# Optimization experiments

Hardware: AMD Instinct MI355X
Metric: run time of the kernel (lower is better)

Reference implementation:

```python
import jax, jax.numpy as jnp
import numpy as np

B, T, E, A = 4, 4096, 512, 64

def setup_inputs() -> dict:
    key = jax.random.key(0)
    k1, k2, k3, k4 = jax.random.split(key, 4)
    embedded = jax.random.normal(k1, (B, T, E), dtype=jnp.float32)
    # torch Linear(E, A, bias=False): weight [A, E], y = x @ W.T. Store as [E, A].
    s = 1.0 / np.sqrt(E)
    Wq = jax.random.uniform(k2, (E, A), dtype=jnp.float32, minval=-s, maxval=s)
    Wk = jax.random.uniform(k3, (E, A), dtype=jnp.float32, minval=-s, maxval=s)
    Wv = jax.random.uniform(k4, (E, A), dtype=jnp.float32, minval=-s, maxval=s)
    return {"embedded": embedded, "Wq": Wq, "Wk": Wk, "Wv": Wv}

def reference(embedded, Wq, Wk, Wv):
    Q = embedded @ Wq  # [B, T, A]
    K = embedded @ Wk
    V = embedded @ Wv
    A_dim = V.shape[-1]
    scores = jnp.einsum('btd,bsd->bts', Q, K) / jnp.sqrt(jnp.float32(A_dim))  # [B, T, T]
    Tlen = scores.shape[-1]
    causal = jnp.tril(jnp.ones((Tlen, Tlen), dtype=bool))
    scores = jnp.where(causal, scores, -jnp.inf)
    attn = jax.nn.softmax(scores, axis=-1)
    out = jnp.einsum('bts,bsd->btd', attn, V)  # [B, T, A]
    return jnp.round(out, 4)
```

## Files before the change

### kernel.cpp

```cpp
#include <hip/hip_runtime.h>

#define B_ 4
#define T_ 4096
#define E_ 512
#define A_ 64
#define SQSCALE 0.1803368801111204f

typedef __attribute__((ext_vector_type(8)))  short bf16x8;
typedef __attribute__((ext_vector_type(8)))  unsigned short ushort8;
typedef __attribute__((ext_vector_type(4)))  unsigned int   u32x4;
typedef __attribute__((ext_vector_type(4)))  float f32x4;
typedef __attribute__((ext_vector_type(16))) float f32x16;

__device__ __forceinline__ unsigned short f2bf(float x) {
    union { float f; unsigned int u; } v; v.f = x;
    unsigned int r = v.u + 0x7fffu + ((v.u >> 16) & 1u);
    return (unsigned short)(r >> 16);
}
__device__ __forceinline__ unsigned cvtpk(float a, float b) {
    unsigned r;
    asm("v_cvt_pk_bf16_f32 %0, %1, %2" : "=v"(r) : "v"(a), "v"(b));
    return r;
}
__device__ __forceinline__ void pls(unsigned &a, unsigned &b) {
    asm("v_permlane32_swap_b32 %0, %1" : "+v"(a), "+v"(b));
}

__global__ __launch_bounds__(256) void prep_w(
    const float* __restrict__ Wq, const float* __restrict__ Wk,
    const float* __restrict__ Wv, unsigned short* __restrict__ Wp)
{
    const int e = blockIdx.x * 256 + threadIdx.x;
    const int nt = e >> 10;
    const int ks = (e >> 6) & 15;
    const int l  = e & 63;
    const int col = nt * 16 + (l & 15);
    const int kb  = ks * 32 + (l >> 4) * 8;
    const float* W = (col < 64) ? Wq : ((col < 128) ? Wk : Wv);
    const int cc = col & 63;
    const float sc = (col < 64) ? SQSCALE : 1.f;
    union { unsigned short s[8]; ushort8 v; } u;
    #pragma unroll
    for (int j = 0; j < 8; ++j) u.s[j] = f2bf(W[(kb + j) * 64 + cc] * sc);
    *(ushort8*)&Wp[(size_t)e * 8] = u.v;
}

__global__ __launch_bounds__(768, 4) void qkv_proj_kernel(
    const float* __restrict__ emb, const unsigned short* __restrict__ Wp,
    unsigned short* __restrict__ Qp, unsigned short* __restrict__ Kp,
    unsigned short* __restrict__ Vp)
{
    __shared__ unsigned short at[32][536];
    __shared__ unsigned short qt[32][72];
    __shared__ unsigned short kt[32][72];
    __shared__ unsigned short vt[64][40];
    const int tid = threadIdx.x;
    const long row0 = (long)blockIdx.x * 32;

    if (tid < 512) {
        const int r = tid >> 4, c16 = tid & 15;
        const float* __restrict__ src = emb + (row0 + r) * 512;
        #pragma unroll
        for (int j = 0; j < 4; ++j) {
            const int col = j * 128 + c16 * 8;
            const float4 x0 = *(const float4*)(src + col);
            const float4 x1 = *(const float4*)(src + col + 4);
            u32x4 p;
            p[0] = cvtpk(x0.x, x0.y); p[1] = cvtpk(x0.z, x0.w);
            p[2] = cvtpk(x1.x, x1.y); p[3] = cvtpk(x1.z, x1.w);
            *(u32x4*)&at[r][col] = p;
        }
    }
    __syncthreads();

    const int w = tid >> 6, lane = tid & 63;
    const int c = lane & 15, hi = lane >> 4;

    f32x4 acc[2];
    acc[0] = (f32x4){0.f, 0.f, 0.f, 0.f};
    acc[1] = (f32x4){0.f, 0.f, 0.f, 0.f};

    #pragma unroll
    for (int ks = 0; ks < 16; ++ks) {
        const bf16x8 bf_ = *(const bf16x8*)&Wp[((size_t)(w * 16 + ks) * 64 + lane) * 8];
        const bf16x8 a0 = *(const bf16x8*)&at[c][ks * 32 + hi * 8];
        const bf16x8 a1 = *(const bf16x8*)&at[16 + c][ks * 32 + hi * 8];
        acc[0] = __builtin_amdgcn_mfma_f32_16x16x32_bf16(a0, bf_, acc[0], 0, 0, 0);
        acc[1] = __builtin_amdgcn_mfma_f32_16x16x32_bf16(a1, bf_, acc[1], 0, 0, 0);
    }

    #pragma unroll
    for (int rr = 0; rr < 2; ++rr)
        #pragma unroll
        for (int r4 = 0; r4 < 4; ++r4) {
            const int rloc = rr * 16 + hi * 4 + r4;
            const unsigned short v = f2bf(acc[rr][r4]);
            if (w < 4)       qt[rloc][w * 16 + c] = v;
            else if (w < 8)  kt[rloc][(w - 4) * 16 + c] = v;
            else             vt[(w - 8) * 16 + c][rloc] = v;
        }
    __syncthreads();

    const int tloc = (int)(row0 & 4095);
    const long bb = row0 >> 12;
    const int ci  = tloc >> 6;
    const int f_  = (tloc >> 5) & 1;
    const int ks0 = (tloc >> 4) & 3;
    const int tt  = tloc >> 5;
    if (tid < 256) {
        const int kk = tid >> 6, l = tid & 63;
        const ushort8 kval = *(const ushort8*)&kt[l & 31][kk * 16 + (l >> 5) * 8];
        *(ushort8*)&Kp[((((bb * 64 + ci) * 2 + f_) * 4 + kk) * 64 + l) * 8] = kval;
        const ushort8 qval = *(const ushort8*)&qt[l & 31][kk * 16 + (l >> 5) * 8];
        *(ushort8*)&Qp[(((bb * 128 + tt) * 4 + kk) * 64 + l) * 8] = qval;
    } else if (tid < 512) {
        const int e = tid - 256;
        const int ksl = e >> 7, ct = (e >> 6) & 1, l = e & 63;
        const ushort8 val = *(const ushort8*)&vt[ct * 32 + (l & 31)][ksl * 16 + (l >> 5) * 8];
        *(ushort8*)&Vp[((((bb * 64 + ci) * 4 + ks0 + ksl) * 2 + ct) * 64 + l) * 8] = val;
    }
}

__global__ __launch_bounds__(512, 1) void attn_kernel(
    const unsigned short* __restrict__ Qp, const unsigned short* __restrict__ Kp,
    const unsigned short* __restrict__ Vp, float* __restrict__ out)
{
    __shared__ float accbuf[8][32][68];
    __shared__ float mbuf[8][32], lbuf[8][32];

    const int tid = threadIdx.x, w = tid >> 6, lane = tid & 63;
    const int c = lane & 31, h = lane >> 5;
    const int b = blockIdx.x & 3;
    const int pp = blockIdx.x >> 2;

    const unsigned short* __restrict__ Qpb = Qp + (size_t)b * 128 * 4 * 512;
    const unsigned short* __restrict__ Kpb = Kp + (size_t)b * 64 * 8 * 512;
    const unsigned short* __restrict__ Vpb = Vp + (size_t)b * 64 * 8 * 512;

    for (int ti = 0; ti < 2; ++ti) {
        const int t = ti ? pp : (127 - pp);
        const int qb = t << 5;
        const int nc = ((qb + 31) >> 6) + 1;

        bf16x8 qf[4];
        #pragma unroll
        for (int kk = 0; kk < 4; ++kk)
            qf[kk] = *(const bf16x8*)&Qpb[(((size_t)t * 4 + kk) * 64 + lane) * 8];

        f32x16 acc[2];
        #pragma unroll
        for (int ct = 0; ct < 2; ++ct)
            #pragma unroll
            for (int j = 0; j < 16; ++j) acc[ct][j] = 0.f;
        float m = -1e30f, l = 0.f;

        const unsigned short* kptr = Kpb + (size_t)w * 4096 + lane * 8;
        const unsigned short* vptr = Vpb + (size_t)w * 4096 + lane * 8;

        bf16x8 kf[2][4];
        {
            const unsigned short* kp0 = (w < nc) ? kptr : (kptr - (size_t)(w - nc + 1) * 4096);
            #pragma unroll
            for (int f = 0; f < 2; ++f)
                #pragma unroll
                for (int kk = 0; kk < 4; ++kk)
                    kf[f][kk] = *(const bf16x8*)&kp0[f * 2048 + kk * 512];
        }

        for (int ci = w; ci < nc; ci += 8) {
            const int s0 = ci << 6;

            bf16x8 vf[4][2];
            #pragma unroll
            for (int ks = 0; ks < 4; ++ks)
                #pragma unroll
                for (int ct = 0; ct < 2; ++ct)
                    vf[ks][ct] = *(const bf16x8*)&vptr[ks * 1024 + ct * 512];

            f32x16 sf[2];
            #pragma unroll
            for (int f = 0; f < 2; ++f)
                #pragma unroll
                for (int j = 0; j < 16; ++j) sf[f][j] = 0.f;
            __builtin_amdgcn_s_setprio(1);
            #pragma unroll
            for (int f = 0; f < 2; ++f)
                #pragma unroll
                for (int kk = 0; kk < 4; ++kk)
                    sf[f] = __builtin_amdgcn_mfma_f32_32x32x16_bf16(kf[f][kk], qf[kk], sf[f], 0, 0, 0);
            __builtin_amdgcn_s_setprio(0);

            const unsigned short* knp = (ci + 8 < nc) ? (kptr + 32768) : kptr;
            bf16x8 kn[2][4];
            #pragma unroll
            for (int f = 0; f < 2; ++f)
                #pragma unroll
                for (int kk = 0; kk < 4; ++kk)
                    kn[f][kk] = *(const bf16x8*)&knp[f * 2048 + kk * 512];

            if (s0 + 63 > qb) {
                #pragma unroll
                for (int f = 0; f < 2; ++f)
                    #pragma unroll
                    for (int r = 0; r < 16; ++r) {
                        const int key = s0 + f * 32 + ((r & 3) + 8 * (r >> 2)) + 4 * h;
                        if (key > qb + c) sf[f][r] = -1e30f;
                    }
            }

            float t0 = fmaxf(sf[0][0], sf[1][0]);
            float t1 = fmaxf(sf[0][1], sf[1][1]);
            float t2 = fmaxf(sf[0][2], sf[1][2]);
            float t3 = fmaxf(sf[0][3], sf[1][3]);
            #pragma unroll
            for (int r = 4; r < 16; r += 4) {
                t0 = fmaxf(t0, fmaxf(sf[0][r],     sf[1][r]));
                t1 = fmaxf(t1, fmaxf(sf[0][r + 1], sf[1][r + 1]));
                t2 = fmaxf(t2, fmaxf(sf[0][r + 2], sf[1][r + 2]));
                t3 = fmaxf(t3, fmaxf(sf[0][r + 3], sf[1][r + 3]));
            }
            float pm = fmaxf(fmaxf(t0, t1), fmaxf(t2, t3));
            pm = fmaxf(pm, __shfl_xor(pm, 32));

            float mn = m;
            if (__any(pm > m)) {
                mn = fmaxf(m, pm);
                const float sc = exp2f(m - mn);
                m = mn;
                l *= sc;
                #pragma unroll
                for (int ct = 0; ct < 2; ++ct)
                    #pragma unroll
                    for (int r = 0; r < 16; ++r) acc[ct][r] *= sc;
            }

            float s0a = 0.f, s1a = 0.f, s2a = 0.f, s3a = 0.f;
            #pragma unroll
            for (int f = 0; f < 2; ++f)
                #pragma unroll
                for (int r = 0; r < 16; r += 4) {
                    float p0 = exp2f(sf[f][r] - mn);
                    float p1 = exp2f(sf[f][r + 1] - mn);
                    float p2 = exp2f(sf[f][r + 2] - mn);
                    float p3 = exp2f(sf[f][r + 3] - mn);
                    sf[f][r] = p0; sf[f][r + 1] = p1; sf[f][r + 2] = p2; sf[f][r + 3] = p3;
                    s0a += p0; s1a += p1; s2a += p2; s3a += p3;
                }
            float rs = (s0a + s1a) + (s2a + s3a);
            rs += __shfl_xor(rs, 32);
            l += rs;

            #pragma unroll
            for (int f = 0; f < 2; ++f) {
                unsigned w01 = cvtpk(sf[f][0], sf[f][1]);
                unsigned w23 = cvtpk(sf[f][2], sf[f][3]);
                unsigned w45 = cvtpk(sf[f][4], sf[f][5]);
                unsigned w67 = cvtpk(sf[f][6], sf[f][7]);
                pls(w01, w45); pls(w23, w67);
                union { unsigned uu[4]; bf16x8 v; } pa0, pa1;
                pa0.uu[0] = w01; pa0.uu[1] = w23; pa0.uu[2] = w45; pa0.uu[3] = w67;
                unsigned x01 = cvtpk(sf[f][8],  sf[f][9]);
                unsigned x23 = cvtpk(sf[f][10], sf[f][11]);
                unsigned x45 = cvtpk(sf[f][12], sf[f][13]);
                unsigned x67 = cvtpk(sf[f][14], sf[f][15]);
                pls(x01, x45); pls(x23, x67);
                pa1.uu[0] = x01; pa1.uu[1] = x23; pa1.uu[2] = x45; pa1.uu[3] = x67;
                __builtin_amdgcn_s_setprio(1);
                #pragma unroll
                for (int ct = 0; ct < 2; ++ct) {
                    acc[ct] = __builtin_amdgcn_mfma_f32_32x32x16_bf16(vf[2 * f][ct],     pa0.v, acc[ct], 0, 0, 0);
                    acc[ct] = __builtin_amdgcn_mfma_f32_32x32x16_bf16(vf[2 * f + 1][ct], pa1.v, acc[ct], 0, 0, 0);
                }
                __builtin_amdgcn_s_setprio(0);
            }

            #pragma unroll
            for (int f = 0; f < 2; ++f)
                #pragma unroll
                for (int kk = 0; kk < 4; ++kk) kf[f][kk] = kn[f][kk];
            kptr += 32768;
            vptr += 32768;
        }

        if (h == 0) { mbuf[w][c] = m; lbuf[w][c] = l; }
        #pragma unroll
        for (int ct = 0; ct < 2; ++ct)
            #pragma unroll
            for (int g = 0; g < 4; ++g)
                *(float4*)&accbuf[w][c][ct * 32 + g * 8 + 4 * h] =
                    make_float4(acc[ct][4 * g], acc[ct][4 * g + 1],
                                acc[ct][4 * g + 2], acc[ct][4 * g + 3]);
        __syncthreads();
        #pragma unroll
        for (int i = 0; i < 4; ++i) {
            const int e = tid + i * 512;
            const int q = e >> 6, d = e & 63;
            float ms = mbuf[0][q];
            #pragma unroll
            for (int wv = 1; wv < 8; ++wv) ms = fmaxf(ms, mbuf[wv][q]);
            float ls = 0.f, os = 0.f;
            #pragma unroll
            for (int wv = 0; wv < 8; ++wv) {
                const float e_ = exp2f(mbuf[wv][q] - ms);
                ls += lbuf[wv][q] * e_;
                os += accbuf[wv][q][d] * e_;
            }
            out[((long)b * T_ + qb + q) * 64 + d] = os / ls;
        }
        __syncthreads();
    }
}

extern "C" void kernel_launch(void* const* d_in, const int* in_sizes, int n_in,
                              void* d_out, int out_size, void* d_ws, size_t ws_size,
                              hipStream_t stream)
{
    const float* emb = (const float*)d_in[0];
    const float* Wq  = (const float*)d_in[1];
    const float* Wk  = (const float*)d_in[2];
    const float* Wv  = (const float*)d_in[3];
    float* out = (float*)d_out;

    unsigned short* Qp = (unsigned short*)d_ws;
    unsigned short* Kp = Qp + (size_t)B_ * T_ * A_;
    unsigned short* Vp = Kp + (size_t)B_ * T_ * A_;
    unsigned short* Wp = Vp + (size_t)B_ * T_ * A_;

    prep_w<<<dim3(48), dim3(256), 0, stream>>>(Wq, Wk, Wv, Wp);
    qkv_proj_kernel<<<dim3(512), dim3(768), 0, stream>>>(emb, Wp, Qp, Kp, Vp);
    attn_kernel<<<dim3(256), dim3(512), 0, stream>>>(Qp, Kp, Vp, out);
}
```

Baseline: 44.73 us.

## Interleave the two paired query tiles' KV loops and allow two blocks per CU

Each block handles two query tiles (a long one and a short one). Previously it processed them one after the other; now it keeps both tiles' state live and runs their KV steps alternately in one loop, so work from the two tiles can overlap and hide latency. The launch bound is also changed from 1 to 2 blocks per CU. Holding two sets of accumulators, Q fragments and K prefetch registers roughly doubles register use, while the new bound asks for half the registers per thread. This risks spills or reduced instruction-level parallelism.

```diff
diff --git a/kernel.cpp b/kernel.cpp
--- a/kernel.cpp
+++ b/kernel.cpp
@@ -121,7 +121,160 @@
     }
 }
 
-__global__ __launch_bounds__(512, 1) void attn_kernel(
+struct TS {
+    const unsigned short* kptr;
+    const unsigned short* vptr;
+    bf16x8 qf[4];
+    bf16x8 kf[2][4];
+    f32x16 acc[2];
+    float m, l;
+    int nc, qb, ci;
+};
+
+__device__ __forceinline__ void tile_init(TS& s, int t,
+    const unsigned short* __restrict__ Qpb, const unsigned short* __restrict__ Kpb,
+    const unsigned short* __restrict__ Vpb, int w, int lane)
+{
+    s.qb = t << 5;
+    s.nc = ((s.qb + 31) >> 6) + 1;
+    #pragma unroll
+    for (int kk = 0; kk < 4; ++kk)
+        s.qf[kk] = *(const bf16x8*)&Qpb[(((size_t)t * 4 + kk) * 64 + lane) * 8];
+    #pragma unroll
+    for (int ct = 0; ct < 2; ++ct)
+        #pragma unroll
+        for (int j = 0; j < 16; ++j) s.acc[ct][j] = 0.f;
+    s.m = -1e30f; s.l = 0.f;
+    s.kptr = Kpb + (size_t)w * 4096 + lane * 8;
+    s.vptr = Vpb + (size_t)w * 4096 + lane * 8;
+    s.ci = w;
+    const unsigned short* kp0 = (w < s.nc) ? s.kptr : (s.kptr - (size_t)(w - s.nc + 1) * 4096);
+    #pragma unroll
+    for (int f = 0; f < 2; ++f)
+        #pragma unroll
+        for (int kk = 0; kk < 4; ++kk)
+            s.kf[f][kk] = *(const bf16x8*)&kp0[f * 2048 + kk * 512];
+}
+
+__device__ __forceinline__ void tile_step(TS& s, int h)
+{
+    const int s0 = s.ci << 6;
+
+    bf16x8 vf[4][2];
+    #pragma unroll
+    for (int ks = 0; ks < 4; ++ks)
+        #pragma unroll
+        for (int ct = 0; ct < 2; ++ct)
+            vf[ks][ct] = *(const bf16x8*)&s.vptr[ks * 1024 + ct * 512];
+
+    f32x16 sf[2];
+    #pragma unroll
+    for (int f = 0; f < 2; ++f)
+        #pragma unroll
+        for (int j = 0; j < 16; ++j) sf[f][j] = 0.f;
+    __builtin_amdgcn_s_setprio(1);
+    #pragma unroll
+    for (int f = 0; f < 2; ++f)
+        #pragma unroll
+        for (int kk = 0; kk < 4; ++kk)
+            sf[f] = __builtin_amdgcn_mfma_f32_32x32x16_bf16(s.kf[f][kk], s.qf[kk], sf[f], 0, 0, 0);
+    __builtin_amdgcn_s_setprio(0);
+
+    const unsigned short* knp = (s.ci + 8 < s.nc) ? (s.kptr + 32768) : s.kptr;
+    bf16x8 kn[2][4];
+    #pragma unroll
+    for (int f = 0; f < 2; ++f)
+        #pragma unroll
+        for (int kk = 0; kk < 4; ++kk)
+            kn[f][kk] = *(const bf16x8*)&knp[f * 2048 + kk * 512];
+
+    const int c = (int)(threadIdx.x & 31);
+    if (s0 + 63 > s.qb) {
+        #pragma unroll
+        for (int f = 0; f < 2; ++f)
+            #pragma unroll
+            for (int r = 0; r < 16; ++r) {
+                const int key = s0 + f * 32 + ((r & 3) + 8 * (r >> 2)) + 4 * h;
+                if (key > s.qb + c) sf[f][r] = -1e30f;
+            }
+    }
+
+    float t0 = fmaxf(sf[0][0], sf[1][0]);
+    float t1 = fmaxf(sf[0][1], sf[1][1]);
+    float t2 = fmaxf(sf[0][2], sf[1][2]);
+    float t3 = fmaxf(sf[0][3], sf[1][3]);
+    #pragma unroll
+    for (int r = 4; r < 16; r += 4) {
+        t0 = fmaxf(t0, fmaxf(sf[0][r],     sf[1][r]));
+        t1 = fmaxf(t1, fmaxf(sf[0][r + 1], sf[1][r + 1]));
+        t2 = fmaxf(t2, fmaxf(sf[0][r + 2], sf[1][r + 2]));
+        t3 = fmaxf(t3, fmaxf(sf[0][r + 3], sf[1][r + 3]));
+    }
+    float pm = fmaxf(fmaxf(t0, t1), fmaxf(t2, t3));
+    pm = fmaxf(pm, __shfl_xor(pm, 32));
+
+    float mn = s.m;
+    if (__any(pm > s.m)) {
+        mn = fmaxf(s.m, pm);
+        const float sc = exp2f(s.m - mn);
+        s.m = mn;
+        s.l *= sc;
+        #pragma unroll
+        for (int ct = 0; ct < 2; ++ct)
+            #pragma unroll
+            for (int r = 0; r < 16; ++r) s.acc[ct][r] *= sc;
+    }
+
+    float s0a = 0.f, s1a = 0.f, s2a = 0.f, s3a = 0.f;
+    #pragma unroll
+    for (int f = 0; f < 2; ++f)
+        #pragma unroll
+        for (int r = 0; r < 16; r += 4) {
+            float p0 = exp2f(sf[f][r] - mn);
+            float p1 = exp2f(sf[f][r + 1] - mn);
+            float p2 = exp2f(sf[f][r + 2] - mn);
+            float p3 = exp2f(sf[f][r + 3] - mn);
+            sf[f][r] = p0; sf[f][r + 1] = p1; sf[f][r + 2] = p2; sf[f][r + 3] = p3;
+            s0a += p0; s1a += p1; s2a += p2; s3a += p3;
+        }
+    float rs = (s0a + s1a) + (s2a + s3a);
+    rs += __shfl_xor(rs, 32);
+    s.l += rs;
+
+    #pragma unroll
+    for (int f = 0; f < 2; ++f) {
+        unsigned w01 = cvtpk(sf[f][0], sf[f][1]);
+        unsigned w23 = cvtpk(sf[f][2], sf[f][3]);
+        unsigned w45 = cvtpk(sf[f][4], sf[f][5]);
+        unsigned w67 = cvtpk(sf[f][6], sf[f][7]);
+        pls(w01, w45); pls(w23, w67);
+        union { unsigned uu[4]; bf16x8 v; } pa0, pa1;
+        pa0.uu[0] = w01; pa0.uu[1] = w23; pa0.uu[2] = w45; pa0.uu[3] = w67;
+        unsigned x01 = cvtpk(sf[f][8],  sf[f][9]);
+        unsigned x23 = cvtpk(sf[f][10], sf[f][11]);
+        unsigned x45 = cvtpk(sf[f][12], sf[f][13]);
+        unsigned x67 = cvtpk(sf[f][14], sf[f][15]);
+        pls(x01, x45); pls(x23, x67);
+        pa1.uu[0] = x01; pa1.uu[1] = x23; pa1.uu[2] = x45; pa1.uu[3] = x67;
+        __builtin_amdgcn_s_setprio(1);
+        #pragma unroll
+        for (int ct = 0; ct < 2; ++ct) {
+            s.acc[ct] = __builtin_amdgcn_mfma_f32_32x32x16_bf16(vf[2 * f][ct],     pa0.v, s.acc[ct], 0, 0, 0);
+            s.acc[ct] = __builtin_amdgcn_mfma_f32_32x32x16_bf16(vf[2 * f + 1][ct], pa1.v, s.acc[ct], 0, 0, 0);
+        }
+        __builtin_amdgcn_s_setprio(0);
+    }
+
+    #pragma unroll
+    for (int f = 0; f < 2; ++f)
+        #pragma unroll
+        for (int kk = 0; kk < 4; ++kk) s.kf[f][kk] = kn[f][kk];
+    s.kptr += 32768;
+    s.vptr += 32768;
+    s.ci += 8;
+}
+
+__global__ __launch_bounds__(512, 2) void attn_kernel(
     const unsigned short* __restrict__ Qp, const unsigned short* __restrict__ Kp,
     const unsigned short* __restrict__ Vp, float* __restrict__ out)
 {
@@ -137,160 +290,40 @@
     const unsigned short* __restrict__ Kpb = Kp + (size_t)b * 64 * 8 * 512;
     const unsigned short* __restrict__ Vpb = Vp + (size_t)b * 64 * 8 * 512;
 
-    for (int ti = 0; ti < 2; ++ti) {
-        const int t = ti ? pp : (127 - pp);
-        const int qb = t << 5;
-        const int nc = ((qb + 31) >> 6) + 1;
-
-        bf16x8 qf[4];
-        #pragma unroll
-        for (int kk = 0; kk < 4; ++kk)
-            qf[kk] = *(const bf16x8*)&Qpb[(((size_t)t * 4 + kk) * 64 + lane) * 8];
-
-        f32x16 acc[2];
-        #pragma unroll
-        for (int ct = 0; ct < 2; ++ct)
-            #pragma unroll
-            for (int j = 0; j < 16; ++j) acc[ct][j] = 0.f;
-        float m = -1e30f, l = 0.f;
-
-        const unsigned short* kptr = Kpb + (size_t)w * 4096 + lane * 8;
-        const unsigned short* vptr = Vpb + (size_t)w * 4096 + lane * 8;
-
-        bf16x8 kf[2][4];
-        {
-            const unsigned short* kp0 = (w < nc) ? kptr : (kptr - (size_t)(w - nc + 1) * 4096);
-            #pragma unroll
-            for (int f = 0; f < 2; ++f)
+    TS A, Bt;
+    tile_init(A,  127 - pp, Qpb, Kpb, Vpb, w, lane);
+    tile_init(Bt, pp,       Qpb, Kpb, Vpb, w, lane);
+    const int itA = (A.nc  > w) ? ((A.nc  - w + 7) >> 3) : 0;
+    const int itB = (Bt.nc > w) ? ((Bt.nc - w + 7) >> 3) : 0;
+
+    for (int i = 0; i < itA; ++i) {
+        tile_step(A, h);
+        if (i < itB) tile_step(Bt, h);
+    }
+
+    #pragma unroll
+    for (int which = 0; which < 2; ++which) {
+        if (which == 0) {
+            if (h == 0) { mbuf[w][c] = A.m; lbuf[w][c] = A.l; }
+            #pragma unroll
+            for (int ct = 0; ct < 2; ++ct)
                 #pragma unroll
-                for (int kk = 0; kk < 4; ++kk)
-                    kf[f][kk] = *(const bf16x8*)&kp0[f * 2048 + kk * 512];
-        }
-
-        for (int ci = w; ci < nc; ci += 8) {
-            const int s0 = ci << 6;
-
-            bf16x8 vf[4][2];
-            #pragma unroll
-            for (int ks = 0; ks < 4; ++ks)
+                for (int g = 0; g < 4; ++g)
+                    *(float4*)&accbuf[w][c][ct * 32 + g * 8 + 4 * h] =
+                        make_float4(A.acc[ct][4 * g], A.acc[ct][4 * g + 1],
+                                    A.acc[ct][4 * g + 2], A.acc[ct][4 * g + 3]);
+        } else {
+            if (h == 0) { mbuf[w][c] = Bt.m; lbuf[w][c] = Bt.l; }
+            #pragma unroll
+            for (int ct = 0; ct < 2; ++ct)
                 #pragma unroll
-                for (int ct = 0; ct < 2; ++ct)
-                    vf[ks][ct] = *(const bf16x8*)&vptr[ks * 1024 + ct * 512];
-
-            f32x16 sf[2];
-            #pragma unroll
-            for (int f = 0; f < 2; ++f)
-                #pragma unroll
-                for (int j = 0; j < 16; ++j) sf[f][j] = 0.f;
-            __builtin_amdgcn_s_setprio(1);
-            #pragma unroll
-            for (int f = 0; f < 2; ++f)
-                #pragma unroll
-                for (int kk = 0; kk < 4; ++kk)
-                    sf[f] = __builtin_amdgcn_mfma_f32_32x32x16_bf16(kf[f][kk], qf[kk], sf[f], 0, 0, 0);
-            __builtin_amdgcn_s_setprio(0);
-
-            const unsigned short* knp = (ci + 8 < nc) ? (kptr + 32768) : kptr;
-            bf16x8 kn[2][4];
-            #pragma unroll
-            for (int f = 0; f < 2; ++f)
-                #pragma unroll
-                for (int kk = 0; kk < 4; ++kk)
-                    kn[f][kk] = *(const bf16x8*)&knp[f * 2048 + kk * 512];
-
-            if (s0 + 63 > qb) {
-                #pragma unroll
-                for (int f = 0; f < 2; ++f)
-                    #pragma unroll
-                    for (int r = 0; r < 16; ++r) {
-                        const int key = s0 + f * 32 + ((r & 3) + 8 * (r >> 2)) + 4 * h;
-                        if (key > qb + c) sf[f][r] = -1e30f;
-                    }
-            }
-
-            float t0 = fmaxf(sf[0][0], sf[1][0]);
-            float t1 = fmaxf(sf[0][1], sf[1][1]);
-            float t2 = fmaxf(sf[0][2], sf[1][2]);
-            float t3 = fmaxf(sf[0][3], sf[1][3]);
-            #pragma unroll
-            for (int r = 4; r < 16; r += 4) {
-                t0 = fmaxf(t0, fmaxf(sf[0][r],     sf[1][r]));
-                t1 = fmaxf(t1, fmaxf(sf[0][r + 1], sf[1][r + 1]));
-                t2 = fmaxf(t2, fmaxf(sf[0][r + 2], sf[1][r + 2]));
-                t3 = fmaxf(t3, fmaxf(sf[0][r + 3], sf[1][r + 3]));
-            }
-            float pm = fmaxf(fmaxf(t0, t1), fmaxf(t2, t3));
-            pm = fmaxf(pm, __shfl_xor(pm, 32));
-
-            float mn = m;
-            if (__any(pm > m)) {
-                mn = fmaxf(m, pm);
-                const float sc = exp2f(m - mn);
-                m = mn;
-                l *= sc;
-                #pragma unroll
-                for (int ct = 0; ct < 2; ++ct)
-                    #pragma unroll
-                    for (int r = 0; r < 16; ++r) acc[ct][r] *= sc;
-            }
-
-            float s0a = 0.f, s1a = 0.f, s2a = 0.f, s3a = 0.f;
-            #pragma unroll
-            for (int f = 0; f < 2; ++f)
-                #pragma unroll
-                for (int r = 0; r < 16; r += 4) {
-                    float p0 = exp2f(sf[f][r] - mn);
-                    float p1 = exp2f(sf[f][r + 1] - mn);
-                    float p2 = exp2f(sf[f][r + 2] - mn);
-                    float p3 = exp2f(sf[f][r + 3] - mn);
-                    sf[f][r] = p0; sf[f][r + 1] = p1; sf[f][r + 2] = p2; sf[f][r + 3] = p3;
-                    s0a += p0; s1a += p1; s2a += p2; s3a += p3;
-                }
-            float rs = (s0a + s1a) + (s2a + s3a);
-            rs += __shfl_xor(rs, 32);
-            l += rs;
-
-            #pragma unroll
-            for (int f = 0; f < 2; ++f) {
-                unsigned w01 = cvtpk(sf[f][0], sf[f][1]);
-                unsigned w23 = cvtpk(sf[f][2], sf[f][3]);
-                unsigned w45 = cvtpk(sf[f][4], sf[f][5]);
-                unsigned w67 = cvtpk(sf[f][6], sf[f][7]);
-                pls(w01, w45); pls(w23, w67);
-                union { unsigned uu[4]; bf16x8 v; } pa0, pa1;
-                pa0.uu[0] = w01; pa0.uu[1] = w23; pa0.uu[2] = w45; pa0.uu[3] = w67;
-                unsigned x01 = cvtpk(sf[f][8],  sf[f][9]);
-                unsigned x23 = cvtpk(sf[f][10], sf[f][11]);
-                unsigned x45 = cvtpk(sf[f][12], sf[f][13]);
-                unsigned x67 = cvtpk(sf[f][14], sf[f][15]);
-                pls(x01, x45); pls(x23, x67);
-                pa1.uu[0] = x01; pa1.uu[1] = x23; pa1.uu[2] = x45; pa1.uu[3] = x67;
-                __builtin_amdgcn_s_setprio(1);
-                #pragma unroll
-                for (int ct = 0; ct < 2; ++ct) {
-                    acc[ct] = __builtin_amdgcn_mfma_f32_32x32x16_bf16(vf[2 * f][ct],     pa0.v, acc[ct], 0, 0, 0);
-                    acc[ct] = __builtin_amdgcn_mfma_f32_32x32x16_bf16(vf[2 * f + 1][ct], pa1.v, acc[ct], 0, 0, 0);
-                }
-                __builtin_amdgcn_s_setprio(0);
-            }
-
-            #pragma unroll
-            for (int f = 0; f < 2; ++f)
-                #pragma unroll
-                for (int kk = 0; kk < 4; ++kk) kf[f][kk] = kn[f][kk];
-            kptr += 32768;
-            vptr += 32768;
-        }
-
-        if (h == 0) { mbuf[w][c] = m; lbuf[w][c] = l; }
-        #pragma unroll
-        for (int ct = 0; ct < 2; ++ct)
-            #pragma unroll
-            for (int g = 0; g < 4; ++g)
-                *(float4*)&accbuf[w][c][ct * 32 + g * 8 + 4 * h] =
-                    make_float4(acc[ct][4 * g], acc[ct][4 * g + 1],
-                                acc[ct][4 * g + 2], acc[ct][4 * g + 3]);
+                for (int g = 0; g < 4; ++g)
+                    *(float4*)&accbuf[w][c][ct * 32 + g * 8 + 4 * h] =
+                        make_float4(Bt.acc[ct][4 * g], Bt.acc[ct][4 * g + 1],
+                                    Bt.acc[ct][4 * g + 2], Bt.acc[ct][4 * g + 3]);
+        }
         __syncthreads();
+        const int qb = which ? (pp << 5) : ((127 - pp) << 5);
         #pragma unroll
         for (int i = 0; i < 4; ++i) {
             const int e = tid + i * 512;
```

Result: slower. 58.30 us (+30.3%).
